# Kernel optimization log

Measured on AMD Instinct MI355X. Metric: run time of the kernel, lower is better.

The kernel has to match this reference:

```python
import jax, jax.numpy as jnp
import numpy as np

N_NODES = 100000
N_EDGES = 1600000
N_GRAPHS = 64
DIMS = [(128, 128), (128, 128), (128, 64)]  # (in, out) per SAGEConv layer


def setup_inputs() -> dict:
    key = jax.random.key(0)
    ks = jax.random.split(key, 16)
    inp = {
        "x": jax.random.normal(ks[0], (N_NODES, DIMS[0][0]), dtype=jnp.float32),
        "edge_index": jax.random.randint(ks[1], (2, N_EDGES), 0, N_NODES, dtype=jnp.int64),
        "batch": jnp.sort(jax.random.randint(ks[2], (N_NODES,), 0, N_GRAPHS, dtype=jnp.int64)),
        "edge_attr": jax.random.normal(ks[3], (N_EDGES, 4), dtype=jnp.float32),
    }
    # SAGEConv params: lin_l (applied to mean-aggregated neighbors, has bias),
    # lin_r (applied to root/self features, no bias) -- PyG defaults.
    for i, (din, dout) in enumerate(DIMS):
        s = 1.0 / np.sqrt(din)
        inp[f"Wl{i}"] = jax.random.normal(ks[4 + 3 * i], (din, dout), dtype=jnp.float32) * s
        inp[f"Wr{i}"] = jax.random.normal(ks[5 + 3 * i], (din, dout), dtype=jnp.float32) * s
        inp[f"b{i}"] = jnp.zeros((dout,), dtype=jnp.float32)
    return inp


def _sage_conv(x, edge_index, Wl, Wr, b):
    # messages flow src -> dst (PyG source_to_target), mean aggregation at dst
    src, dst = edge_index[0], edge_index[1]
    msg = x[src]  # [E, F] gather
    agg = jax.ops.segment_sum(msg, dst, num_segments=x.shape[0])  # [N, F]
    deg = jax.ops.segment_sum(jnp.ones((src.shape[0],), x.dtype), dst, num_segments=x.shape[0])
    agg = agg / jnp.maximum(deg, 1.0)[:, None]  # mean; isolated nodes -> 0
    return agg @ Wl + x @ Wr + b


def reference(x, edge_index, batch, edge_attr, Wl0, Wr0, b0, Wl1, Wr1, b1, Wl2, Wr2, b2):
    del edge_attr  # cast to float in original, never used by SAGEConv
    h = x.astype(jnp.float32)
    params = [(Wl0, Wr0, b0), (Wl1, Wr1, b1), (Wl2, Wr2, b2)]
    for i, (Wl, Wr, b) in enumerate(params):
        h = _sage_conv(h, edge_index, Wl, Wr, b)
        if i < len(params) - 1:
            h = jax.nn.relu(h)  # dropout is identity in eval mode
    # global_mean_pool over graphs
    pooled = jax.ops.segment_sum(h, batch, num_segments=N_GRAPHS)
    counts = jax.ops.segment_sum(jnp.ones((h.shape[0],), h.dtype), batch, num_segments=N_GRAPHS)
    return pooled / jnp.maximum(counts, 1.0)[:, None]
```

## Files before the change

### kernel.cpp

```cpp
#include <hip/hip_runtime.h>
#include <hip/hip_bf16.h>

#define NN 100000
#define NE 1600000
#define NG 64
#define NBUK 782
#define ABLK 512
#define ACH 3125
#define PSPLIT 8

typedef short short8 __attribute__((ext_vector_type(8)));
typedef float f32x4 __attribute__((ext_vector_type(4)));
typedef float f32x2 __attribute__((ext_vector_type(2)));
typedef unsigned short ushort8v __attribute__((ext_vector_type(8)));
typedef unsigned int uint4v __attribute__((ext_vector_type(4)));
typedef unsigned int uint2v __attribute__((ext_vector_type(2)));

static inline int cdiv(int a, int b) { return (a + b - 1) / b; }

__device__ __forceinline__ short f2bf(float f) {
    return __builtin_bit_cast(short, __float2bfloat16(f));
}
__device__ __forceinline__ float bf2f(unsigned short u) {
    unsigned int x = ((unsigned int)u) << 16;
    return __builtin_bit_cast(float, x);
}

__global__ __launch_bounds__(256) void xcvt_kernel(const float* __restrict__ x,
                                                   short* __restrict__ xb, int n8) {
    int i = blockIdx.x * 256 + threadIdx.x;
    if (i >= n8) return;
    const float4 v0 = ((const float4*)x)[i * 2];
    const float4 v1 = ((const float4*)x)[i * 2 + 1];
    short8 o;
    o[0] = f2bf(v0.x); o[1] = f2bf(v0.y); o[2] = f2bf(v0.z); o[3] = f2bf(v0.w);
    o[4] = f2bf(v1.x); o[5] = f2bf(v1.y); o[6] = f2bf(v1.z); o[7] = f2bf(v1.w);
    ((short8*)xb)[i] = o;
}

__global__ __launch_bounds__(256) void histA_kernel(const int* __restrict__ dst,
                                                    int* __restrict__ blockHist, int E) {
    __shared__ int h[NBUK];
    for (int i = threadIdx.x; i < NBUK; i += 256) h[i] = 0;
    __syncthreads();
    int base = blockIdx.x * ACH;
    int end = min(base + ACH, E);
    for (int e = base + threadIdx.x; e < end; e += 256) atomicAdd(&h[dst[e] >> 7], 1);
    __syncthreads();
    for (int i = threadIdx.x; i < NBUK; i += 256) blockHist[(size_t)i * ABLK + blockIdx.x] = h[i];
}

__global__ __launch_bounds__(512) void scanBlk_kernel(int* __restrict__ blockHist,
                                                      int* __restrict__ bucketTot) {
    __shared__ int s[ABLK];
    int b = blockIdx.x, t = threadIdx.x;
    int v = blockHist[(size_t)b * ABLK + t];
    s[t] = v;
    __syncthreads();
    for (int o = 1; o < ABLK; o <<= 1) {
        int u = (t >= o) ? s[t - o] : 0;
        __syncthreads();
        s[t] += u;
        __syncthreads();
    }
    blockHist[(size_t)b * ABLK + t] = s[t] - v;
    if (t == ABLK - 1) bucketTot[b] = s[ABLK - 1];
}

__global__ __launch_bounds__(1024) void scanTot_kernel(const int* __restrict__ bucketTot,
                                                       int* __restrict__ bucketBase,
                                                       int* __restrict__ off, int E) {
    __shared__ int s[1024];
    int t = threadIdx.x;
    int v = (t < NBUK) ? bucketTot[t] : 0;
    s[t] = v;
    __syncthreads();
    for (int o = 1; o < 1024; o <<= 1) {
        int u = (t >= o) ? s[t - o] : 0;
        __syncthreads();
        s[t] += u;
        __syncthreads();
    }
    if (t < NBUK) bucketBase[t] = s[t] - v;
    if (t == 0) {
        bucketBase[NBUK] = E;
        off[NN] = E;
    }
}

__global__ __launch_bounds__(256) void binA_kernel(const int* __restrict__ src,
                                                   const int* __restrict__ dst,
                                                   const int* __restrict__ blockHist,
                                                   const int* __restrict__ bucketBase,
                                                   int* __restrict__ binned, int E) {
    __shared__ int cur[NBUK];
    __shared__ int lbase[NBUK];
    for (int i = threadIdx.x; i < NBUK; i += 256) {
        cur[i] = 0;
        lbase[i] = bucketBase[i] + blockHist[(size_t)i * ABLK + blockIdx.x];
    }
    __syncthreads();
    int base = blockIdx.x * ACH;
    int end = min(base + ACH, E);
    for (int e = base + threadIdx.x; e < end; e += 256) {
        int d = dst[e];
        int b = d >> 7;
        int r = atomicAdd(&cur[b], 1);
        binned[lbase[b] + r] = src[e] | ((d & 127) << 20);
    }
}

__global__ __launch_bounds__(256) void bucketB_kernel(const int* __restrict__ binned,
                                                      const int* __restrict__ bucketBase,
                                                      int* __restrict__ csr,
                                                      int* __restrict__ off,
                                                      float* __restrict__ ideg, int N) {
    __shared__ int pair[2048];
    __shared__ int stage[4096];
    __shared__ int deg[128], loff[128], cur[128];
    int b = blockIdx.x, t = threadIdx.x;
    int e0 = bucketBase[b], e1 = bucketBase[b + 1];
    int cnt = e1 - e0;
    if (t < 128) deg[t] = 0;
    __syncthreads();
    for (int c0 = 0; c0 < cnt; c0 += 2048) {
        int cc = min(2048, cnt - c0);
        for (int i = t; i < cc; i += 256) pair[i] = binned[e0 + c0 + i];
        __syncthreads();
        for (int i = t; i < cc; i += 256) atomicAdd(&deg[pair[i] >> 20], 1);
        __syncthreads();
    }
    if (t < 128) loff[t] = deg[t];
    __syncthreads();
    for (int o = 1; o < 128; o <<= 1) {
        int u = (t < 128 && t >= o) ? loff[t - o] : 0;
        __syncthreads();
        if (t < 128) loff[t] += u;
        __syncthreads();
    }
    int nodeBase = b * 128;
    if (t < 128) {
        int ex = loff[t] - deg[t];
        cur[t] = ex;
        int n = nodeBase + t;
        if (n < N) {
            off[n] = e0 + ex;
            ideg[n] = 1.0f / (float)max(deg[t], 1);
        }
    }
    __syncthreads();
    if (cnt <= 4096) {
        for (int c0 = 0; c0 < cnt; c0 += 2048) {
            int cc = min(2048, cnt - c0);
            for (int i = t; i < cc; i += 256) pair[i] = binned[e0 + c0 + i];
            __syncthreads();
            for (int i = t; i < cc; i += 256) {
                int p = pair[i];
                int r = atomicAdd(&cur[p >> 20], 1);
                stage[r] = p & 0xFFFFF;
            }
            __syncthreads();
        }
        for (int i = t; i < cnt; i += 256) csr[e0 + i] = stage[i];
    } else {
        for (int c0 = 0; c0 < cnt; c0 += 2048) {
            int cc = min(2048, cnt - c0);
            for (int i = t; i < cc; i += 256) pair[i] = binned[e0 + c0 + i];
            __syncthreads();
            for (int i = t; i < cc; i += 256) {
                int p = pair[i];
                int r = atomicAdd(&cur[p >> 20], 1);
                csr[e0 + r] = p & 0xFFFFF;
            }
            __syncthreads();
        }
    }
}

template <int OUT>
__global__ void wt_kernel(const float* __restrict__ Wl, const float* __restrict__ Wr,
                          short* __restrict__ WT) {
    int idx = blockIdx.x * 256 + threadIdx.x;
    if (idx >= 2 * OUT * 128) return;
    int c = idx >> 7, k = idx & 127;
    float v = (c < OUT) ? Wl[k * OUT + c] : Wr[k * OUT + (c - OUT)];
    WT[idx] = f2bf(v);
}

template <int OUT>
__global__ __launch_bounds__(256) void sage_gemm_mfma(
    const short* __restrict__ h, const short* __restrict__ WT,
    const float* __restrict__ bias,
    unsigned char* __restrict__ P, short* __restrict__ Q, int N) {
    constexpr int K = 128;
    constexpr int NT = OUT / 32;
    constexpr int WC = OUT / 2;
    constexpr int PWP = WC / 4 + 4;
    constexpr int PWQ = WC / 2 + 4;
    constexpr int LDSB = 32 * PWQ * 4;

    __shared__ char ldsAll[4 * LDSB];

    const int tid = threadIdx.x;
    const int w = tid >> 6;
    const int lane = tid & 63;
    const int l15 = lane & 15;
    const int lhi = lane >> 4;
    const int rowBase = blockIdx.x * 64;
    const int colBase = w * WC;
    const bool isQ = (w >= 2);
    const int ocolBase = isQ ? colBase - OUT : colBase;
    char* myL = ldsAll + w * LDSB;

    f32x4 acc[4][NT];
#pragma unroll
    for (int mt = 0; mt < 4; ++mt)
#pragma unroll
        for (int nt = 0; nt < NT; ++nt) acc[mt][nt] = (f32x4){0.f, 0.f, 0.f, 0.f};

#pragma unroll
    for (int kt = 0; kt < 4; ++kt) {
        const int k0 = kt * 32 + lhi * 8;
        short8 a[4], b[NT];
#pragma unroll
        for (int mt = 0; mt < 4; ++mt) {
            int r = rowBase + mt * 16 + l15;
            r = min(r, N - 1);
            a[mt] = *(const short8*)(h + (size_t)r * K + k0);
        }
#pragma unroll
        for (int nt = 0; nt < NT; ++nt)
            b[nt] = *(const short8*)(WT + (size_t)(colBase + nt * 16 + l15) * K + k0);
#pragma unroll
        for (int mt = 0; mt < 4; ++mt)
#pragma unroll
            for (int nt = 0; nt < NT; ++nt)
                acc[mt][nt] = __builtin_amdgcn_mfma_f32_16x16x32_bf16(b[nt], a[mt], acc[mt][nt], 0, 0, 0);
    }

    if (!isQ) {
        constexpr int LPR = WC / 16;
        constexpr int RPP = 64 / LPR;
        constexpr int NP = 32 / RPP;
#pragma unroll
        for (int hh = 0; hh < 2; ++hh) {
#pragma unroll
            for (int mt2 = 0; mt2 < 2; ++mt2) {
                int mt = hh * 2 + mt2;
                int lr = mt2 * 16 + l15;
#pragma unroll
                for (int nt = 0; nt < NT; ++nt) {
                    unsigned u = (unsigned)__builtin_amdgcn_cvt_pk_fp8_f32(
                        acc[mt][nt][0], acc[mt][nt][1], 0, false);
                    u = (unsigned)__builtin_amdgcn_cvt_pk_fp8_f32(
                        acc[mt][nt][2], acc[mt][nt][3], (int)u, true);
                    *(unsigned*)(myL + (size_t)(lr * PWP + nt * 4 + lhi) * 4) = u;
                }
            }
#pragma unroll
            for (int p2 = 0; p2 < NP; ++p2) {
                int lr = p2 * RPP + lane / LPR;
                int wc = (lane % LPR) * 4;
                uint4v v = *(uint4v*)(myL + (size_t)(lr * PWP + wc) * 4);
                int grow = rowBase + hh * 32 + lr;
                if (grow < N)
                    *(uint4v*)(P + (size_t)grow * OUT + ocolBase + wc * 4) = v;
            }
        }
    } else {
        float4 bj[NT];
#pragma unroll
        for (int nt = 0; nt < NT; ++nt)
            bj[nt] = *(const float4*)(bias + ocolBase + nt * 16 + lhi * 4);
        constexpr int LPR = WC / 8;
        constexpr int RPP = 64 / LPR;
        constexpr int NP = 32 / RPP;
#pragma unroll
        for (int hh = 0; hh < 2; ++hh) {
#pragma unroll
            for (int mt2 = 0; mt2 < 2; ++mt2) {
                int mt = hh * 2 + mt2;
                int lr = mt2 * 16 + l15;
#pragma unroll
                for (int nt = 0; nt < NT; ++nt) {
                    float v0 = acc[mt][nt][0] + bj[nt].x;
                    float v1 = acc[mt][nt][1] + bj[nt].y;
                    float v2 = acc[mt][nt][2] + bj[nt].z;
                    float v3 = acc[mt][nt][3] + bj[nt].w;
                    unsigned lo = ((unsigned)(unsigned short)f2bf(v0)) |
                                  ((unsigned)(unsigned short)f2bf(v1) << 16);
                    unsigned hi = ((unsigned)(unsigned short)f2bf(v2)) |
                                  ((unsigned)(unsigned short)f2bf(v3) << 16);
                    uint2v u; u[0] = lo; u[1] = hi;
                    *(uint2v*)(myL + (size_t)(lr * PWQ + (nt * 4 + lhi) * 2) * 4) = u;
                }
            }
#pragma unroll
            for (int p2 = 0; p2 < NP; ++p2) {
                int lr = p2 * RPP + lane / LPR;
                int wc = (lane % LPR) * 4;
                uint4v v = *(uint4v*)(myL + (size_t)(lr * PWQ + wc) * 4);
                int grow = rowBase + hh * 32 + lr;
                if (grow < N)
                    *(uint4v*)((unsigned short*)Q + (size_t)grow * OUT + ocolBase + (lane % LPR) * 8) = v;
            }
        }
    }
}

template <int F, bool RELU>
__global__ __launch_bounds__(256) void gather_kernel(
    const int* __restrict__ csr, const int* __restrict__ off,
    const unsigned char* __restrict__ P, const float* __restrict__ ideg,
    const short* __restrict__ Qin, short* __restrict__ hout, int N) {
    constexpr int C = F / 16;
    int t = blockIdx.x * blockDim.x + threadIdx.x;
    int n = t / C, c = t % C;
    if (n >= N) return;
    int e0 = off[n], e1 = off[n + 1];
    const size_t cb = (size_t)c * 16;

    float f[16];
#pragma unroll
    for (int j = 0; j < 16; ++j) f[j] = 0.f;

    int e = e0;
    for (; e + 4 <= e1; e += 4) {
        int s0 = csr[e + 0], s1 = csr[e + 1], s2 = csr[e + 2], s3 = csr[e + 3];
        uint4v u0 = *(const uint4v*)(P + (size_t)s0 * F + cb);
        uint4v u1 = *(const uint4v*)(P + (size_t)s1 * F + cb);
        uint4v u2 = *(const uint4v*)(P + (size_t)s2 * F + cb);
        uint4v u3 = *(const uint4v*)(P + (size_t)s3 * F + cb);
#pragma unroll
        for (int wd = 0; wd < 4; ++wd) {
            f32x2 a0 = __builtin_amdgcn_cvt_pk_f32_fp8(u0[wd], false);
            f32x2 b0 = __builtin_amdgcn_cvt_pk_f32_fp8(u0[wd], true);
            f32x2 a1 = __builtin_amdgcn_cvt_pk_f32_fp8(u1[wd], false);
            f32x2 b1 = __builtin_amdgcn_cvt_pk_f32_fp8(u1[wd], true);
            f32x2 a2 = __builtin_amdgcn_cvt_pk_f32_fp8(u2[wd], false);
            f32x2 b2 = __builtin_amdgcn_cvt_pk_f32_fp8(u2[wd], true);
            f32x2 a3 = __builtin_amdgcn_cvt_pk_f32_fp8(u3[wd], false);
            f32x2 b3 = __builtin_amdgcn_cvt_pk_f32_fp8(u3[wd], true);
            f[wd * 4 + 0] += (a0[0] + a1[0]) + (a2[0] + a3[0]);
            f[wd * 4 + 1] += (a0[1] + a1[1]) + (a2[1] + a3[1]);
            f[wd * 4 + 2] += (b0[0] + b1[0]) + (b2[0] + b3[0]);
            f[wd * 4 + 3] += (b0[1] + b1[1]) + (b2[1] + b3[1]);
        }
    }
    for (; e < e1; ++e) {
        uint4v u = *(const uint4v*)(P + (size_t)csr[e] * F + cb);
#pragma unroll
        for (int wd = 0; wd < 4; ++wd) {
            f32x2 a = __builtin_amdgcn_cvt_pk_f32_fp8(u[wd], false);
            f32x2 b = __builtin_amdgcn_cvt_pk_f32_fp8(u[wd], true);
            f[wd * 4 + 0] += a[0];
            f[wd * 4 + 1] += a[1];
            f[wd * 4 + 2] += b[0];
            f[wd * 4 + 3] += b[1];
        }
    }

    float sc = ideg[n];
    const short* qp = Qin + (size_t)n * F + cb;
    ushort8v qa = *(const ushort8v*)qp, qb = *(const ushort8v*)(qp + 8);
    short8 oa, ob;
#pragma unroll
    for (int j = 0; j < 8; ++j) {
        float va = fmaf(f[j], sc, bf2f(qa[j]));
        float vb = fmaf(f[j + 8], sc, bf2f(qb[j]));
        if (RELU) { va = fmaxf(va, 0.f); vb = fmaxf(vb, 0.f); }
        oa[j] = f2bf(va);
        ob[j] = f2bf(vb);
    }
    short* op = hout + (size_t)n * F + cb;
    *(short8*)op = oa;
    *(short8*)(op + 8) = ob;
}

__global__ __launch_bounds__(256) void gbound_kernel(const int* __restrict__ batch,
                                                     int* __restrict__ gstart, int N) {
    int n = blockIdx.x * 256 + threadIdx.x;
    if (n >= N) return;
    int b = batch[n];
    if (n == 0) {
        for (int g = 0; g <= b; ++g) gstart[g] = 0;
    } else {
        int pb = batch[n - 1];
        for (int g = pb + 1; g <= b; ++g) gstart[g] = n;
    }
    if (n == N - 1) {
        for (int g = b + 1; g <= NG; ++g) gstart[g] = N;
    }
}

__global__ __launch_bounds__(256) void pool2_kernel(const unsigned short* __restrict__ h,
                                                    const int* __restrict__ gstart,
                                                    float* __restrict__ gpart) {
    int g = blockIdx.x / PSPLIT, part = blockIdx.x % PSPLIT;
    int s = gstart[g], e = gstart[g + 1];
    int cnt = e - s;
    int chunk = (cnt + PSPLIT - 1) / PSPLIT;
    int n0 = s + part * chunk;
    int n1 = min(n0 + chunk, e);
    int j = threadIdx.x & 63;
    int r = threadIdx.x >> 6;
    float acc = 0.f;
    for (int n = n0 + r; n < n1; n += 4) acc += bf2f(h[(size_t)n * 64 + j]);
    __shared__ float ls[256];
    ls[threadIdx.x] = acc;
    __syncthreads();
    if (threadIdx.x < 64) {
        float v = ls[threadIdx.x] + ls[threadIdx.x + 64] + ls[threadIdx.x + 128] + ls[threadIdx.x + 192];
        gpart[(size_t)(g * PSPLIT + part) * 64 + threadIdx.x] = v;
    }
}

__global__ void final_kernel(const float* __restrict__ gpart, const int* __restrict__ gstart,
                             float* __restrict__ out) {
    int t = blockIdx.x * blockDim.x + threadIdx.x;
    if (t >= NG * 64) return;
    int g = t >> 6, j = t & 63;
    float s = 0.f;
#pragma unroll
    for (int p = 0; p < PSPLIT; ++p) s += gpart[(size_t)(g * PSPLIT + p) * 64 + j];
    int cnt = gstart[g + 1] - gstart[g];
    out[t] = s / (float)max(cnt, 1);
}

extern "C" void kernel_launch(void* const* d_in, const int* in_sizes, int n_in,
                              void* d_out, int out_size, void* d_ws, size_t ws_size,
                              hipStream_t stream) {
    const float* x     = (const float*)d_in[0];
    const int*   ei    = (const int*)d_in[1];
    const int*   batch = (const int*)d_in[2];
    const float* Wl0 = (const float*)d_in[4];
    const float* Wr0 = (const float*)d_in[5];
    const float* b0  = (const float*)d_in[6];
    const float* Wl1 = (const float*)d_in[7];
    const float* Wr1 = (const float*)d_in[8];
    const float* b1  = (const float*)d_in[9];
    const float* Wl2 = (const float*)d_in[10];
    const float* Wr2 = (const float*)d_in[11];
    const float* b2  = (const float*)d_in[12];

    const int N = NN, E = NE;
    const int* src = ei;
    const int* dst = ei + E;

    const size_t HB = (size_t)NN * 128 * 2;
    char* ws = (char*)d_ws;
    short* xbf  = (short*)(ws);
    short* hA   = (short*)(ws + HB);
    short* hB   = (short*)(ws + 2 * HB);
    short* bufQ = (short*)(ws + 3 * HB);
    unsigned char* bufP = (unsigned char*)(ws + 4 * HB);
    char* p = ws + 4 * HB + (size_t)NN * 128;
    short* WT0  = (short*)p;        p += 256 * 128 * 2;
    short* WT1  = (short*)p;        p += 256 * 128 * 2;
    short* WT2  = (short*)p;        p += 128 * 128 * 2;
    float* ideg = (float*)p;        p += (size_t)N * 4;
    int* off    = (int*)p;          p += (size_t)(N + 4) * 4;
    int* blockHist = (int*)p;       p += (size_t)NBUK * ABLK * 4 + 16;
    int* bucketTot = (int*)p;       p += 784 * 4;
    int* bucketBase= (int*)p;       p += 784 * 4;
    int* gstart = (int*)p;          p += (NG + 2) * 4;
    float* gpart = (float*)p;       p += (size_t)NG * PSPLIT * 64 * 4;
    int* binned = (int*)p;          p += (size_t)E * 4;
    int* csr    = (int*)p;          p += (size_t)E * 4;

    histA_kernel<<<ABLK, 256, 0, stream>>>(dst, blockHist, E);
    scanBlk_kernel<<<NBUK, ABLK, 0, stream>>>(blockHist, bucketTot);
    scanTot_kernel<<<1, 1024, 0, stream>>>(bucketTot, bucketBase, off, E);
    binA_kernel<<<ABLK, 256, 0, stream>>>(src, dst, blockHist, bucketBase, binned, E);
    bucketB_kernel<<<NBUK, 256, 0, stream>>>(binned, bucketBase, csr, off, ideg, N);

    wt_kernel<128><<<cdiv(2 * 128 * 128, 256), 256, 0, stream>>>(Wl0, Wr0, WT0);
    wt_kernel<128><<<cdiv(2 * 128 * 128, 256), 256, 0, stream>>>(Wl1, Wr1, WT1);
    wt_kernel<64><<<cdiv(2 * 64 * 128, 256), 256, 0, stream>>>(Wl2, Wr2, WT2);
    xcvt_kernel<<<cdiv(N * 128 / 8, 256), 256, 0, stream>>>(x, xbf, N * 128 / 8);
    gbound_kernel<<<cdiv(N, 256), 256, 0, stream>>>(batch, gstart, N);

    const int GB = cdiv(N, 64);

    sage_gemm_mfma<128><<<GB, 256, 0, stream>>>(xbf, WT0, b0, bufP, bufQ, N);
    gather_kernel<128, true><<<cdiv(N * 8, 256), 256, 0, stream>>>(csr, off, bufP, ideg, bufQ, hA, N);
    sage_gemm_mfma<128><<<GB, 256, 0, stream>>>(hA, WT1, b1, bufP, bufQ, N);
    gather_kernel<128, true><<<cdiv(N * 8, 256), 256, 0, stream>>>(csr, off, bufP, ideg, bufQ, hB, N);
    sage_gemm_mfma<64><<<GB, 256, 0, stream>>>(hB, WT2, b2, bufP, bufQ, N);
    gather_kernel<64, false><<<cdiv(N * 4, 256), 256, 0, stream>>>(csr, off, bufP, ideg, bufQ, hA, N);

    pool2_kernel<<<NG * PSPLIT, 256, 0, stream>>>((const unsigned short*)hA, gstart, gpart);
    final_kernel<<<16, 256, 0, stream>>>(gpart, gstart, (float*)d_out);
}
```

Baseline: 275.4 us.

## Fuse setup kernels into one launch and stage GEMM A-tile through swizzled LDS

Five small setup kernels become a single launch that dispatches work by block index: x conversion to bf16, the three weight transposes, and graph boundary detection. This removes four kernel launches and the gaps between them. The SAGE GEMM now copies its 64x128 bf16 A tile into LDS with global_load_lds, using an XOR swizzle, and reads its MFMA operands from LDS instead of from global memory. The last block no longer clamps row indices, so it reads past the final row of the activation buffer.

```diff
diff --git a/kernel.cpp b/kernel.cpp
--- a/kernel.cpp
+++ b/kernel.cpp
@@ -24,18 +24,6 @@
 __device__ __forceinline__ float bf2f(unsigned short u) {
     unsigned int x = ((unsigned int)u) << 16;
     return __builtin_bit_cast(float, x);
-}
-
-__global__ __launch_bounds__(256) void xcvt_kernel(const float* __restrict__ x,
-                                                   short* __restrict__ xb, int n8) {
-    int i = blockIdx.x * 256 + threadIdx.x;
-    if (i >= n8) return;
-    const float4 v0 = ((const float4*)x)[i * 2];
-    const float4 v1 = ((const float4*)x)[i * 2 + 1];
-    short8 o;
-    o[0] = f2bf(v0.x); o[1] = f2bf(v0.y); o[2] = f2bf(v0.z); o[3] = f2bf(v0.w);
-    o[4] = f2bf(v1.x); o[5] = f2bf(v1.y); o[6] = f2bf(v1.z); o[7] = f2bf(v1.w);
-    ((short8*)xb)[i] = o;
 }
 
 __global__ __launch_bounds__(256) void histA_kernel(const int* __restrict__ dst,
@@ -177,14 +165,49 @@
     }
 }
 
-template <int OUT>
-__global__ void wt_kernel(const float* __restrict__ Wl, const float* __restrict__ Wr,
-                          short* __restrict__ WT) {
-    int idx = blockIdx.x * 256 + threadIdx.x;
-    if (idx >= 2 * OUT * 128) return;
+__device__ __forceinline__ void wt_body(const float* Wl, const float* Wr, short* WT,
+                                        int OUT, int idx) {
     int c = idx >> 7, k = idx & 127;
     float v = (c < OUT) ? Wl[k * OUT + c] : Wr[k * OUT + (c - OUT)];
     WT[idx] = f2bf(v);
+}
+
+__global__ __launch_bounds__(256) void setup_kernel(
+    const float* __restrict__ x, short* __restrict__ xb,
+    const float* __restrict__ Wl0, const float* __restrict__ Wr0, short* __restrict__ WT0,
+    const float* __restrict__ Wl1, const float* __restrict__ Wr1, short* __restrict__ WT1,
+    const float* __restrict__ Wl2, const float* __restrict__ Wr2, short* __restrict__ WT2,
+    const int* __restrict__ batch, int* __restrict__ gstart) {
+    int b = blockIdx.x;
+    int tid = threadIdx.x;
+    if (b < 6250) {
+        int i = b * 256 + tid;
+        const float4 v0 = ((const float4*)x)[i * 2];
+        const float4 v1 = ((const float4*)x)[i * 2 + 1];
+        short8 o;
+        o[0] = f2bf(v0.x); o[1] = f2bf(v0.y); o[2] = f2bf(v0.z); o[3] = f2bf(v0.w);
+        o[4] = f2bf(v1.x); o[5] = f2bf(v1.y); o[6] = f2bf(v1.z); o[7] = f2bf(v1.w);
+        ((short8*)xb)[i] = o;
+    } else if (b < 6378) {
+        wt_body(Wl0, Wr0, WT0, 128, (b - 6250) * 256 + tid);
+    } else if (b < 6506) {
+        wt_body(Wl1, Wr1, WT1, 128, (b - 6378) * 256 + tid);
+    } else if (b < 6570) {
+        wt_body(Wl2, Wr2, WT2, 64, (b - 6506) * 256 + tid);
+    } else {
+        int n = (b - 6570) * 256 + tid;
+        if (n >= NN) return;
+        int g1 = batch[n];
+        if (n == 0) {
+            for (int g = 0; g <= g1; ++g) gstart[g] = 0;
+        } else {
+            int pb = batch[n - 1];
+            for (int g = pb + 1; g <= g1; ++g) gstart[g] = n;
+        }
+        if (n == NN - 1) {
+            for (int g = g1 + 1; g <= NG; ++g) gstart[g] = NN;
+        }
+    }
 }
 
 template <int OUT>
@@ -199,7 +222,8 @@
     constexpr int PWQ = WC / 2 + 4;
     constexpr int LDSB = 32 * PWQ * 4;
 
-    __shared__ char ldsAll[4 * LDSB];
+    __shared__ char As[16384];
+    __shared__ char eLds[4 * LDSB];
 
     const int tid = threadIdx.x;
     const int w = tid >> 6;
@@ -210,7 +234,23 @@
     const int colBase = w * WC;
     const bool isQ = (w >= 2);
     const int ocolBase = isQ ? colBase - OUT : colBase;
-    char* myL = ldsAll + w * LDSB;
+    char* myL = eLds + w * LDSB;
+
+    {
+        const char* gsrc = (const char*)(h + (size_t)rowBase * K);
+#pragma unroll
+        for (int p = 0; p < 4; ++p) {
+            int lbase = (w * 4 + p) * 1024;
+            int loff = lbase + lane * 16;
+            int row = loff >> 8;
+            int scol = (loff & 255) ^ ((row & 7) << 4);
+            __builtin_amdgcn_global_load_lds(
+                (const __attribute__((address_space(1))) unsigned int*)(gsrc + (size_t)row * 256 + scol),
+                (__attribute__((address_space(3))) unsigned int*)(As + lbase),
+                16, 0, 0);
+        }
+    }
+    __syncthreads();
 
     f32x4 acc[4][NT];
 #pragma unroll
@@ -220,17 +260,16 @@
 
 #pragma unroll
     for (int kt = 0; kt < 4; ++kt) {
-        const int k0 = kt * 32 + lhi * 8;
+        const int kb = kt * 64 + lhi * 16;
         short8 a[4], b[NT];
 #pragma unroll
         for (int mt = 0; mt < 4; ++mt) {
-            int r = rowBase + mt * 16 + l15;
-            r = min(r, N - 1);
-            a[mt] = *(const short8*)(h + (size_t)r * K + k0);
+            int row = mt * 16 + l15;
+            a[mt] = *(const short8*)(As + row * 256 + (kb ^ ((row & 7) << 4)));
         }
 #pragma unroll
         for (int nt = 0; nt < NT; ++nt)
-            b[nt] = *(const short8*)(WT + (size_t)(colBase + nt * 16 + l15) * K + k0);
+            b[nt] = *(const short8*)(WT + (size_t)(colBase + nt * 16 + l15) * K + kt * 32 + lhi * 8);
 #pragma unroll
         for (int mt = 0; mt < 4; ++mt)
 #pragma unroll
@@ -375,22 +414,6 @@
     short* op = hout + (size_t)n * F + cb;
     *(short8*)op = oa;
     *(short8*)(op + 8) = ob;
-}
-
-__global__ __launch_bounds__(256) void gbound_kernel(const int* __restrict__ batch,
-                                                     int* __restrict__ gstart, int N) {
-    int n = blockIdx.x * 256 + threadIdx.x;
-    if (n >= N) return;
-    int b = batch[n];
-    if (n == 0) {
-        for (int g = 0; g <= b; ++g) gstart[g] = 0;
-    } else {
-        int pb = batch[n - 1];
-        for (int g = pb + 1; g <= b; ++g) gstart[g] = n;
-    }
-    if (n == N - 1) {
-        for (int g = b + 1; g <= NG; ++g) gstart[g] = N;
-    }
 }
 
 __global__ __launch_bounds__(256) void pool2_kernel(const unsigned short* __restrict__ h,
@@ -474,11 +497,8 @@
     binA_kernel<<<ABLK, 256, 0, stream>>>(src, dst, blockHist, bucketBase, binned, E);
     bucketB_kernel<<<NBUK, 256, 0, stream>>>(binned, bucketBase, csr, off, ideg, N);
 
-    wt_kernel<128><<<cdiv(2 * 128 * 128, 256), 256, 0, stream>>>(Wl0, Wr0, WT0);
-    wt_kernel<128><<<cdiv(2 * 128 * 128, 256), 256, 0, stream>>>(Wl1, Wr1, WT1);
-    wt_kernel<64><<<cdiv(2 * 64 * 128, 256), 256, 0, stream>>>(Wl2, Wr2, WT2);
-    xcvt_kernel<<<cdiv(N * 128 / 8, 256), 256, 0, stream>>>(x, xbf, N * 128 / 8);
-    gbound_kernel<<<cdiv(N, 256), 256, 0, stream>>>(batch, gstart, N);
+    setup_kernel<<<6961, 256, 0, stream>>>(x, xbf, Wl0, Wr0, WT0, Wl1, Wr1, WT1,
+                                           Wl2, Wr2, WT2, batch, gstart);
 
     const int GB = cdiv(N, 64);
 
```

Measured after the change: 243.7 us. 11.5% less time.
